# Optimization experiments

Hardware: AMD Instinct MI355X
Metric: run time of the kernel (lower is better)

The kernel has to match this reference:

```python
import jax, jax.numpy as jnp
import numpy as np
import math

B, T = 512, 512
ENC = 512          # 2 * input_size
N_MELS, R = 80, 2
ATTN, DEC = 256, 256
PRE_H, PRE_O = 256, 256
HID = 128          # DCA hidden
SC, SK = 8, 21     # static channels / kernel
DC, DK = 8, 21     # dynamic channels / kernel
PL, PA, PB = 11, 0.1, 0.9  # prior length, alpha, beta


def _betabinom_pmf(k, n, a, b):
    lg = math.lgamma
    return math.exp(lg(n + 1) - lg(k + 1) - lg(n - k + 1)
                    + lg(k + a) + lg(n - k + b) - lg(n + a + b)
                    - (lg(a) + lg(b) - lg(a + b)))


def setup_inputs() -> dict:
    key = jax.random.key(0)
    ks = iter(jax.random.split(key, 64))
    def rn(shape, s=0.05):
        return jax.random.normal(next(ks), shape, dtype=jnp.float32) * s
    inp = {}
    inp["h"] = rn([B, T, ENC], 1.0)
    inp["y"] = rn([B, N_MELS], 1.0)
    a = jax.random.uniform(next(ks), [B, T], dtype=jnp.float32)
    inp["alpha"] = a / a.sum(-1, keepdims=True)  # valid attention distribution
    inp["c"] = rn([B, ENC], 1.0)
    for n in ["attn_h0", "attn_c0", "rnn1_h0", "rnn1_c0", "rnn2_h0", "rnn2_c0"]:
        inp[n] = rn([B, ATTN], 1.0)
    # prenet
    inp["fc1_w"] = rn([PRE_H, N_MELS]); inp["fc1_b"] = rn([PRE_H])
    inp["fc2_w"] = rn([PRE_O, PRE_H]); inp["fc2_b"] = rn([PRE_O])
    # dynamic convolution attention
    inp["W_w"] = rn([HID, ATTN]); inp["W_b"] = rn([HID])
    inp["V_w"] = rn([DC * DK, HID])
    inp["F_w"] = rn([SC, 1, SK])
    inp["U_w"] = rn([HID, SC])
    inp["T_w"] = rn([HID, DC]); inp["T_b"] = rn([HID])
    inp["v_w"] = rn([1, HID])
    P = np.array([_betabinom_pmf(k, PL - 1, PA, PB) for k in range(PL)], np.float32)[::-1].copy()
    inp["P"] = jnp.asarray(P)
    # attn LSTM cell: input = 2*input_size + prenet output = 768
    inp["attn_wih"] = rn([4 * ATTN, ENC + PRE_O]); inp["attn_whh"] = rn([4 * ATTN, ATTN])
    inp["attn_bih"] = rn([4 * ATTN]); inp["attn_bhh"] = rn([4 * ATTN])
    inp["lin_w"] = rn([DEC, ENC + ATTN]); inp["lin_b"] = rn([DEC])
    for pfx in ["r1", "r2"]:
        inp[pfx + "_wih"] = rn([4 * DEC, DEC]); inp[pfx + "_whh"] = rn([4 * DEC, DEC])
        inp[pfx + "_bih"] = rn([4 * DEC]); inp[pfx + "_bhh"] = rn([4 * DEC])
    inp["proj_w"] = rn([N_MELS * R, DEC])
    return inp


def _lstm(x, h, c, wih, whh, bih, bhh):
    g = x @ wih.T + bih + h @ whh.T + bhh
    i, f, gg, o = jnp.split(g, 4, axis=-1)
    c2 = jax.nn.sigmoid(f) * c + jax.nn.sigmoid(i) * jnp.tanh(gg)
    return jax.nn.sigmoid(o) * jnp.tanh(c2), c2


def _win(x, k):
    # x: [B, T + k - 1] padded signal -> sliding windows [B, T, k]
    idx = jnp.arange(T)[:, None] + jnp.arange(k)[None, :]
    return x[:, idx]


def reference(h, y, alpha, c, attn_h0, attn_c0, rnn1_h0, rnn1_c0, rnn2_h0, rnn2_c0,
              fc1_w, fc1_b, fc2_w, fc2_b, W_w, W_b, V_w, F_w, U_w, T_w, T_b, v_w, P,
              attn_wih, attn_whh, attn_bih, attn_bhh, lin_w, lin_b,
              r1_wih, r1_whh, r1_bih, r1_bhh, r2_wih, r2_whh, r2_bih, r2_bhh, proj_w):
    # prenet (eval mode -> dropout inactive since fixed=False)
    yp = jax.nn.relu(jax.nn.relu(y @ fc1_w.T + fc1_b) @ fc2_w.T + fc2_b)
    attn_h, attn_c = _lstm(jnp.concatenate([c, yp], -1), attn_h0, attn_c0,
                           attn_wih, attn_whh, attn_bih, attn_bhh)
    # --- dynamic convolution attention ---
    # prior: causal conv with flipped beta-binomial pmf
    p = jnp.einsum('btk,k->bt', _win(jnp.pad(alpha, ((0, 0), (PL - 1, 0))), PL), P)
    p = jnp.log(jnp.clip(p, 1e-6))
    # dynamic filters per batch element: [B, DC, DK]
    G = (jnp.tanh(attn_h @ W_w.T + W_b) @ V_w.T).reshape(-1, DC, DK)
    wd = _win(jnp.pad(alpha, ((0, 0), ((DK - 1) // 2, (DK - 1) // 2))), DK)  # [B,T,DK]
    g = jnp.einsum('btk,bck->btc', wd, G)  # grouped conv1d, groups=B
    ws = _win(jnp.pad(alpha, ((0, 0), ((SK - 1) // 2, (SK - 1) // 2))), SK)
    f = jnp.einsum('btk,ck->btc', ws, F_w[:, 0, :])  # static conv1d
    e = jnp.squeeze(jnp.tanh(f @ U_w.T + g @ T_w.T + T_b) @ v_w.T, -1) + p
    alpha2 = jax.nn.softmax(e, axis=-1)
    # --- context + decoder stack ---
    c2 = jnp.einsum('bt,btd->bd', alpha2, h)
    x = jnp.concatenate([c2, attn_h], -1) @ lin_w.T + lin_b
    r1_h, r1_c = _lstm(x, rnn1_h0, rnn1_c0, r1_wih, r1_whh, r1_bih, r1_bhh)
    x = x + r1_h
    r2_h, r2_c = _lstm(x, rnn2_h0, rnn2_c0, r2_wih, r2_whh, r2_bih, r2_bhh)
    x = x + r2_h
    out = (x @ proj_w.T).reshape(-1, N_MELS, R)
    return (out, alpha2, c2, attn_h, attn_c, r1_h, r1_c, r2_h, r2_c)
```

## Files before the change

### kernel.cpp

```cpp
#include <hip/hip_runtime.h>

typedef unsigned short u16;
typedef __attribute__((ext_vector_type(8))) short s8v;
typedef __attribute__((ext_vector_type(4))) float f32x4;

__device__ __forceinline__ float bf2f(u16 u) { return __uint_as_float(((unsigned)u) << 16); }
__device__ __forceinline__ u16 f2bf(float f) {
    unsigned u = __float_as_uint(f);
    return (u16)((u + 0x7fffu + ((u >> 16) & 1u)) >> 16);
}
__device__ __forceinline__ float ldraw(const void* p, size_t i, int dt) {
    return dt ? ((const float*)p)[i] : bf2f(((const u16*)p)[i]);
}
__device__ __forceinline__ int fl(const int* F, int f) {
    return f == -1 ? 1 : (f == -2 ? 0 : F[f]);
}
__device__ __forceinline__ float fast_tanh(float x) {
    x = fminf(fmaxf(x, -15.f), 15.f);
    float e = __expf(2.f * x);
    return (e - 1.f) / (e + 1.f);
}
__device__ __forceinline__ float sigm(float x) { return 1.f / (1.f + __expf(-x)); }

__global__ __launch_bounds__(256) void k_detect(int* __restrict__ flagsRaw,
    const void* p0, const void* p1, const void* p2, const void* p3, const void* p4,
    const void* p5, const void* p6, const void* p7, const void* p8, const void* p9,
    const void* p10, const void* p11, const void* p12, const void* p13, const void* p14,
    const void* p15, const void* p16, const void* p17, const void* p18, const void* p19,
    const void* p20, const void* p21, const void* p22, const void* p23, const void* p24,
    const void* p25, const void* p26, const void* p27, const void* p28, const void* p29,
    const void* p30, const void* p31, const void* p32, const void* p33, const void* p34,
    const void* p35, const void* p36, const void* p37)
{
    const void* ptrs[38] = {p0,p1,p2,p3,p4,p5,p6,p7,p8,p9,p10,p11,p12,p13,p14,p15,p16,
                            p17,p18,p19,p20,p21,p22,p23,p24,p25,p26,p27,p28,p29,p30,p31,
                            p32,p33,p34,p35,p36,p37};
    const int ns[38] = {134217728, 40960, 262144, 262144,
                        131072,131072,131072,131072,131072,131072,
                        20480,256,65536,256,
                        32768,128,21504,168,1024,1024,128,128,11,
                        786432,262144,1024,1024, 196608,256,
                        262144,262144,1024,1024, 262144,262144,1024,1024, 40960};
    __shared__ int s;
    int b = blockIdx.x, tid = threadIdx.x;
    if (tid == 0) s = 0;
    __syncthreads();
    int nsamp = ns[b] >> 1;
    if (nsamp > 512) nsamp = 512;
    const u16* q = (const u16*)ptrs[b];
    int bad = 0;
    for (int i = tid; i < nsamp; i += 256) {
        u16 u = q[2 * i];
        int e = (u >> 7) & 0xff;
        bad += (e < 96 || e > 159) ? 1 : 0;
    }
    atomicAdd(&s, bad);
    __syncthreads();
    if (tid == 0) flagsRaw[b] = (s * 4 > nsamp) ? 1 : 0;
}

__global__ __launch_bounds__(256) void k_finish(
    const int* __restrict__ FRAW, int* __restrict__ FF,
    const void* a_wih, const void* a_whh, const void* r1_wih, const void* r1_whh,
    const void* r2_wih, const void* r2_whh,
    const void* U_w, const void* T_w, const void* T_b, const void* v_w, const void* F_w,
    u16* wihA, u16* whhA, u16* w1i, u16* w1h, u16* w2i, u16* w2h,
    float* utw, float* tbf, float* vf, float* ff)
{
    __shared__ int sflag[38];
    const int big[38] = {1,1,1,1, 1,1,1,1,1,1, 1,0,1,0,
                         1,0,1,0,1,1,0,0,0, 1,1,1,1, 1,0,
                         1,1,1,1, 1,1,1,1, 1};
    int tid = threadIdx.x;
    if (tid == 0) {
        int s = 0, c = 0;
        for (int i = 0; i < 38; i++) if (big[i]) { s += FRAW[i]; c++; }
        int maj = (s * 2 > c) ? 1 : 0;
        for (int i = 0; i < 38; i++) sflag[i] = big[i] ? FRAW[i] : maj;
        if (blockIdx.x == 0)
            for (int i = 0; i < 38; i++) FF[i] = sflag[i];
    }
    __syncthreads();

    if (blockIdx.x == 0) {
        int dU = sflag[18], dT = sflag[19], dTb = sflag[20], dV = sflag[21], dF = sflag[17];
        for (int i = tid; i < 1024; i += 256) {
            int j = i >> 3, c = i & 7;
            utw[j * 16 + c]     = ldraw(U_w, i, dU);
            utw[j * 16 + 8 + c] = ldraw(T_w, i, dT);
        }
        if (tid < 128) { tbf[tid] = ldraw(T_b, tid, dTb); vf[tid] = ldraw(v_w, tid, dV); }
        if (tid < 168) ff[tid] = ldraw(F_w, tid, dF);
    }

    const void* srcs[6] = {a_wih, a_whh, r1_wih, r1_whh, r2_wih, r2_whh};
    u16* dsts[6] = {wihA, whhA, w1i, w1h, w2i, w2h};
    const int nsg[6] = {786432, 262144, 262144, 262144, 262144, 262144};
    const int fsg[6] = {23, 24, 29, 30, 33, 34};
    int gtid = blockIdx.x * 256 + tid;
    int gstride = 2048 * 256;
    #pragma unroll
    for (int sgi = 0; sgi < 6; sgi++) {
        int nq = nsg[sgi] >> 2;
        int dt = sflag[fsg[sgi]];
        u16* dst = dsts[sgi];
        if (dt) {
            const float4* src = (const float4*)srcs[sgi];
            for (int q = gtid; q < nq; q += gstride) {
                float4 v = src[q];
                ushort4 o;
                o.x = f2bf(v.x); o.y = f2bf(v.y); o.z = f2bf(v.z); o.w = f2bf(v.w);
                *(ushort4*)&dst[q * 4] = o;
            }
        } else {
            const ushort4* src = (const ushort4*)srcs[sgi];
            for (int q = gtid; q < nq; q += gstride)
                *(ushort4*)&dst[q * 4] = src[q];
        }
    }
}

__device__ __forceinline__ void vg32_pair(const int* F,
    const void* A, int lda, int fa, const void* B, int ldb, int bo, int fb, int K,
    int m0, int n0, int N, int tid, int tx, int ty, float* acc,
    float (*As)[68], float (*Bs)[68])
{
    int dA = fl(F, fa), dB = fl(F, fb);
    bool fastp = dA && dB;
    for (int k0 = 0; k0 < K; k0 += 64) {
        __syncthreads();
        if (fastp) {
            #pragma unroll
            for (int p = 0; p < 2; p++) {
                int e = tid + p * 256;
                int row = e >> 4, kk = (e & 15) * 4;
                float4 va = {0.f, 0.f, 0.f, 0.f};
                if (k0 + kk < K)
                    va = *(const float4*)((const float*)A + (size_t)(m0 + row) * lda + k0 + kk);
                *(float4*)&As[row][kk] = va;
                int nr = n0 + row;
                float4 vb = {0.f, 0.f, 0.f, 0.f};
                if (nr < N && k0 + kk < K)
                    vb = *(const float4*)((const float*)B + (size_t)nr * ldb + bo + k0 + kk);
                *(float4*)&Bs[row][kk] = vb;
            }
        } else {
            #pragma unroll
            for (int p = 0; p < 8; p++) {
                int e = tid + p * 256;
                int row = e >> 6, kk = e & 63;
                As[row][kk] = (k0 + kk < K) ? ldraw(A, (size_t)(m0 + row) * lda + k0 + kk, dA) : 0.f;
                int nr = n0 + row;
                Bs[row][kk] = (nr < N && k0 + kk < K)
                            ? ldraw(B, (size_t)nr * ldb + bo + k0 + kk, dB) : 0.f;
            }
        }
        __syncthreads();
        #pragma unroll
        for (int kq = 0; kq < 16; kq++) {
            float4 a0 = *(const float4*)&As[ty][kq * 4];
            float4 a1 = *(const float4*)&As[ty + 16][kq * 4];
            float4 b0 = *(const float4*)&Bs[tx][kq * 4];
            float4 b1 = *(const float4*)&Bs[tx + 16][kq * 4];
            acc[0] += a0.x*b0.x + a0.y*b0.y + a0.z*b0.z + a0.w*b0.w;
            acc[1] += a0.x*b1.x + a0.y*b1.y + a0.z*b1.z + a0.w*b1.w;
            acc[2] += a1.x*b0.x + a1.y*b0.y + a1.z*b0.z + a1.w*b0.w;
            acc[3] += a1.x*b1.x + a1.y*b1.y + a1.z*b1.z + a1.w*b1.w;
        }
    }
}

__global__ __launch_bounds__(256) void k_vgemm32(
    const int* __restrict__ F,
    const void* A1, int lda1, int fa1, const void* B1, int ldb1, int bo1, int fb1, int K1,
    const void* A2, int lda2, int fa2, const void* B2, int ldb2, int bo2, int fb2, int K2,
    const void* bias1, int fx1,
    float* __restrict__ Cf, int ldc, int N, int act)
{
    __shared__ float As[32][68], Bs[32][68];
    int tid = threadIdx.x, tx = tid & 15, ty = tid >> 4;
    int m0 = blockIdx.y * 32, n0 = blockIdx.x * 32;
    float acc[4] = {0.f, 0.f, 0.f, 0.f};
    vg32_pair(F, A1, lda1, fa1, B1, ldb1, bo1, fb1, K1, m0, n0, N, tid, tx, ty, acc, As, Bs);
    if (A2) vg32_pair(F, A2, lda2, fa2, B2, ldb2, bo2, fb2, K2, m0, n0, N, tid, tx, ty, acc, As, Bs);

    #pragma unroll
    for (int c = 0; c < 2; c++) {
        int n = n0 + tx + c * 16;
        if (n >= N) continue;
        float bias = 0.f;
        if (bias1) bias += ldraw(bias1, n, fl(F, fx1));
        #pragma unroll
        for (int r = 0; r < 2; r++) {
            float v = acc[r * 2 + c] + bias;
            if (act == 1) v = fmaxf(v, 0.f);
            else if (act == 2) v = fast_tanh(v);
            Cf[(size_t)(m0 + ty + r * 16) * ldc + n] = v;
        }
    }
}

__global__ __launch_bounds__(256) void k_lin(
    const int* __restrict__ F, const float* __restrict__ part, float* __restrict__ o_c2,
    const float* __restrict__ ah, const void* lin_w, const void* lin_b,
    float* __restrict__ x1f)
{
    __shared__ float As[32][68], Bs[32][68];
    int tid = threadIdx.x, tx = tid & 15, ty = tid >> 4;
    int m0 = blockIdx.y * 32, n0 = blockIdx.x * 32;
    int dB = fl(F, 27);
    float acc[4] = {0.f, 0.f, 0.f, 0.f};
    for (int k0 = 0; k0 < 512; k0 += 64) {
        __syncthreads();
        #pragma unroll
        for (int p = 0; p < 2; p++) {
            int e = tid + p * 256;
            int row = e >> 4, kk = (e & 15) * 4;
            size_t idx = (size_t)(m0 + row) * 512 + k0 + kk;
            float4 va = *(const float4*)(part + idx);
            float4 vb2 = *(const float4*)(part + idx + 262144);
            va.x += vb2.x; va.y += vb2.y; va.z += vb2.z; va.w += vb2.w;
            *(float4*)&As[row][kk] = va;
            if (blockIdx.x == 0) *(float4*)(o_c2 + idx) = va;
            int nr = n0 + row;
            float4 vb;
            if (dB) {
                vb = *(const float4*)((const float*)lin_w + (size_t)nr * 768 + k0 + kk);
            } else {
                const u16* q = (const u16*)lin_w + (size_t)nr * 768 + k0 + kk;
                vb.x = bf2f(q[0]); vb.y = bf2f(q[1]); vb.z = bf2f(q[2]); vb.w = bf2f(q[3]);
            }
            *(float4*)&Bs[row][kk] = vb;
        }
        __syncthreads();
        #pragma unroll
        for (int kq = 0; kq < 16; kq++) {
            float4 a0 = *(const float4*)&As[ty][kq * 4];
            float4 a1 = *(const float4*)&As[ty + 16][kq * 4];
            float4 b0 = *(const float4*)&Bs[tx][kq * 4];
            float4 b1 = *(const float4*)&Bs[tx + 16][kq * 4];
            acc[0] += a0.x*b0.x + a0.y*b0.y + a0.z*b0.z + a0.w*b0.w;
            acc[1] += a0.x*b1.x + a0.y*b1.y + a0.z*b1.z + a0.w*b1.w;
            acc[2] += a1.x*b0.x + a1.y*b0.y + a1.z*b0.z + a1.w*b0.w;
            acc[3] += a1.x*b1.x + a1.y*b1.y + a1.z*b1.z + a1.w*b1.w;
        }
    }
    vg32_pair(F, ah, 256, -1, lin_w, 768, 512, 27, 256, m0, n0, 256, tid, tx, ty, acc, As, Bs);

    int dbias = fl(F, 28);
    #pragma unroll
    for (int c = 0; c < 2; c++) {
        int n = n0 + tx + c * 16;
        float bias = ldraw(lin_b, n, dbias);
        #pragma unroll
        for (int r = 0; r < 2; r++)
            x1f[(size_t)(m0 + ty + r * 16) * 256 + n] = acc[r * 2 + c] + bias;
    }
}

__device__ __forceinline__ void lstm_mfma_piece(const int* F,
    const void* A, int lda, int fa, const void* B, int ldb, int bo, int fb, int K,
    int b0, int j0, int tid, int wave, int lane, f32x4& acc,
    u16 (*As)[72], u16 (*Bs)[72])
{
    int dA = fl(F, fa), dB = fl(F, fb);
    for (int k0 = 0; k0 < K; k0 += 64) {
        __syncthreads();
        for (int g = tid; g < 640; g += 256) {
            const void* src; int dt; size_t idx; u16* dst;
            if (g < 128) {
                int row = g >> 3, kg = (g & 7) * 8;
                idx = (size_t)(b0 + row) * lda + k0 + kg;
                src = A; dt = dA; dst = &As[row][kg];
            } else {
                int gb = g - 128;
                int row = gb >> 3, kg = (gb & 7) * 8;
                int grow = (row >> 4) * 256 + j0 + (row & 15);
                idx = (size_t)grow * ldb + bo + k0 + kg;
                src = B; dt = dB; dst = &Bs[row][kg];
            }
            if (dt) {
                const float* sp = (const float*)src + idx;
                float4 a = *(const float4*)sp;
                float4 b = *(const float4*)(sp + 4);
                s8v v;
                v[0] = (short)f2bf(a.x); v[1] = (short)f2bf(a.y);
                v[2] = (short)f2bf(a.z); v[3] = (short)f2bf(a.w);
                v[4] = (short)f2bf(b.x); v[5] = (short)f2bf(b.y);
                v[6] = (short)f2bf(b.z); v[7] = (short)f2bf(b.w);
                *(s8v*)dst = v;
            } else {
                *(s8v*)dst = *(const s8v*)((const u16*)src + idx);
            }
        }
        __syncthreads();
        int r = lane & 15, kg = (lane >> 4) * 8;
        s8v a0 = *(const s8v*)&As[r][kg];
        s8v w0 = *(const s8v*)&Bs[wave * 16 + r][kg];
        acc = __builtin_amdgcn_mfma_f32_16x16x32_bf16(a0, w0, acc, 0, 0, 0);
        s8v a1 = *(const s8v*)&As[r][32 + kg];
        s8v w1 = *(const s8v*)&Bs[wave * 16 + r][32 + kg];
        acc = __builtin_amdgcn_mfma_f32_16x16x32_bf16(a1, w1, acc, 0, 0, 0);
    }
}

__global__ __launch_bounds__(256) void k_lstm(
    const int* __restrict__ F,
    const void* A1, int lda1, int fa1, const void* B1, int ldb1, int bo1, int fb1, int K1,
    const void* A2, int lda2, int fa2, const void* B2, int ldb2, int bo2, int fb2, int K2,
    const void* A3, int lda3, int fa3, const void* B3, int ldb3, int bo3, int fb3, int K3,
    const void* bih, int fx1, const void* bhh, int fx2,
    const void* c0, int fc0,
    float* __restrict__ h_out, float* __restrict__ c_out,
    const float* __restrict__ xprev, float* __restrict__ xout)
{
    __shared__ u16 As[16][72];
    __shared__ u16 Bs[64][72];
    __shared__ float sG[4][16][16];
    int tid = threadIdx.x, lane = tid & 63, wave = tid >> 6;
    int j0 = blockIdx.x * 16, b0 = blockIdx.y * 16;
    f32x4 acc = {0.f, 0.f, 0.f, 0.f};
    lstm_mfma_piece(F, A1, lda1, fa1, B1, ldb1, bo1, fb1, K1, b0, j0, tid, wave, lane, acc, As, Bs);
    if (A2) lstm_mfma_piece(F, A2, lda2, fa2, B2, ldb2, bo2, fb2, K2, b0, j0, tid, wave, lane, acc, As, Bs);
    if (A3) lstm_mfma_piece(F, A3, lda3, fa3, B3, ldb3, bo3, fb3, K3, b0, j0, tid, wave, lane, acc, As, Bs);

    #pragma unroll
    for (int r2 = 0; r2 < 4; r2++)
        sG[wave][(lane >> 4) * 4 + r2][lane & 15] = acc[r2];
    __syncthreads();

    int jl = tid & 15, bl = tid >> 4;
    int j = j0 + jl, b = b0 + bl;
    int dx1 = fl(F, fx1), dx2 = fl(F, fx2);
    float gi = sG[0][bl][jl] + ldraw(bih, j, dx1)       + ldraw(bhh, j, dx2);
    float gf = sG[1][bl][jl] + ldraw(bih, j + 256, dx1) + ldraw(bhh, j + 256, dx2);
    float gg = sG[2][bl][jl] + ldraw(bih, j + 512, dx1) + ldraw(bhh, j + 512, dx2);
    float go = sG[3][bl][jl] + ldraw(bih, j + 768, dx1) + ldraw(bhh, j + 768, dx2);
    size_t idx = (size_t)b * 256 + j;
    float cp = ldraw(c0, idx, F[fc0]);
    float cn = sigm(gf) * cp + sigm(gi) * fast_tanh(gg);
    float hn = sigm(go) * fast_tanh(cn);
    h_out[idx] = hn;
    c_out[idx] = cn;
    if (xprev) xout[idx] = xprev[idx] + hn;
}

__global__ __launch_bounds__(256) void k_dca(
    const int* __restrict__ F, const void* __restrict__ alpha, const void* __restrict__ P,
    const float* __restrict__ G, const float* __restrict__ utw, const float* __restrict__ tbf,
    const float* __restrict__ vf, const float* __restrict__ ff,
    float* __restrict__ o_a2)
{
    __shared__ float sFC[16][512];
    __shared__ float sal[532];
    __shared__ float spv[512];
    __shared__ float se[512];
    __shared__ float sff[168], sgd[168];
    __shared__ float sred[8];
    int dA = F[2], dP = F[22];
    int b = blockIdx.x, tid = threadIdx.x;
    if (tid < 168) { sff[tid] = ff[tid]; sgd[tid] = G[(size_t)b * 168 + tid]; }
    for (int i = tid; i < 532; i += 256)
        sal[i] = (i >= 10 && i < 522) ? ldraw(alpha, (size_t)b * 512 + i - 10, dA) : 0.f;
    float pfv[11];
    #pragma unroll
    for (int k = 0; k < 11; k++) pfv[k] = ldraw(P, k, dP);
    __syncthreads();

    #pragma unroll
    for (int q = 0; q < 2; q++) {
        int t = tid + q * 256;
        float aw[21];
        #pragma unroll
        for (int k = 0; k < 21; k++) aw[k] = sal[t + k];
        float pv = 0.f;
        #pragma unroll
        for (int k = 0; k < 11; k++) pv += aw[k] * pfv[k];
        spv[t] = pv;
        #pragma unroll
        for (int c = 0; c < 8; c++) {
            float s1 = 0.f, s2 = 0.f;
            #pragma unroll
            for (int k = 0; k < 21; k++) {
                s1 += aw[k] * sff[c * 21 + k];
                s2 += aw[k] * sgd[c * 21 + k];
            }
            sFC[c][t] = s1;
            sFC[8 + c][t] = s2;
        }
    }
    __syncthreads();

    int js = tid & 31, tg = tid >> 5;
    float4 uu[16];
    {
        const float4* up = (const float4*)(utw + js * 64);
        #pragma unroll
        for (int r = 0; r < 16; r++) uu[r] = up[r];
    }
    float tb4[4], v4[4];
    #pragma unroll
    for (int r = 0; r < 4; r++) { tb4[r] = tbf[js * 4 + r]; v4[r] = vf[js * 4 + r]; }

    for (int tt = 0; tt < 64; tt++) {
        int t = tg * 64 + tt;
        float fc2[8], gc2[8];
        #pragma unroll
        for (int c = 0; c < 8; c++) { fc2[c] = sFC[c][t]; gc2[c] = sFC[8 + c][t]; }
        float ep = 0.f;
        #pragma unroll
        for (int r = 0; r < 4; r++) {
            float4 u0 = uu[r * 4 + 0], u1 = uu[r * 4 + 1];
            float4 t0 = uu[r * 4 + 2], t1 = uu[r * 4 + 3];
            float a = tb4[r];
            a += fc2[0]*u0.x + fc2[1]*u0.y + fc2[2]*u0.z + fc2[3]*u0.w;
            a += fc2[4]*u1.x + fc2[5]*u1.y + fc2[6]*u1.z + fc2[7]*u1.w;
            a += gc2[0]*t0.x + gc2[1]*t0.y + gc2[2]*t0.z + gc2[3]*t0.w;
            a += gc2[4]*t1.x + gc2[5]*t1.y + gc2[6]*t1.z + gc2[7]*t1.w;
            ep += fast_tanh(a) * v4[r];
        }
        #pragma unroll
        for (int off = 16; off >= 1; off >>= 1) ep += __shfl_xor(ep, off);
        if (js == 0) se[t] = ep;
    }
    __syncthreads();

    float e0 = se[tid]       + __logf(fmaxf(spv[tid], 1e-6f));
    float e1 = se[tid + 256] + __logf(fmaxf(spv[tid + 256], 1e-6f));
    float m = fmaxf(e0, e1);
    #pragma unroll
    for (int off = 32; off >= 1; off >>= 1) m = fmaxf(m, __shfl_xor(m, off));
    if ((tid & 63) == 0) sred[tid >> 6] = m;
    __syncthreads();
    m = fmaxf(fmaxf(sred[0], sred[1]), fmaxf(sred[2], sred[3]));
    float x0 = __expf(e0 - m), x1 = __expf(e1 - m);
    float s = x0 + x1;
    #pragma unroll
    for (int off = 32; off >= 1; off >>= 1) s += __shfl_xor(s, off);
    if ((tid & 63) == 0) sred[4 + (tid >> 6)] = s;
    __syncthreads();
    s = sred[4] + sred[5] + sred[6] + sred[7];
    float inv = 1.f / s;
    o_a2[(size_t)b * 512 + tid]       = x0 * inv;
    o_a2[(size_t)b * 512 + tid + 256] = x1 * inv;
}

__global__ __launch_bounds__(256) void k_c2_part(
    const int* __restrict__ F, const float* __restrict__ a2,
    const void* __restrict__ h, float* __restrict__ part)
{
    int dH = F[0];
    int bi = blockIdx.x;
    int b = bi >> 1, sp = bi & 1;
    int tid = threadIdx.x;
    int dsub = (tid & 63) * 8;
    int tsub = tid >> 6;
    __shared__ float sa[256];
    sa[tid] = a2[(size_t)b * 512 + sp * 256 + tid];
    __syncthreads();
    float acc[8];
    #pragma unroll
    for (int j = 0; j < 8; j++) acc[j] = 0.f;
    size_t rowbase = (size_t)b * 512 + sp * 256;
    if (dH) {
        const float* hf = (const float*)h;
        for (int tt = tsub; tt < 256; tt += 4) {
            float a = sa[tt];
            const float* p = hf + (rowbase + tt) * 512 + dsub;
            float4 v0 = *(const float4*)p, v1 = *(const float4*)(p + 4);
            acc[0] += a * v0.x; acc[1] += a * v0.y; acc[2] += a * v0.z; acc[3] += a * v0.w;
            acc[4] += a * v1.x; acc[5] += a * v1.y; acc[6] += a * v1.z; acc[7] += a * v1.w;
        }
    } else {
        const u16* hb = (const u16*)h;
        for (int tt = tsub; tt < 256; tt += 4) {
            float a = sa[tt];
            const u16* p = hb + (rowbase + tt) * 512 + dsub;
            #pragma unroll
            for (int j = 0; j < 8; j++) acc[j] += a * bf2f(p[j]);
        }
    }
    __shared__ float sacc[256 * 8];
    #pragma unroll
    for (int j = 0; j < 8; j++) sacc[tid * 8 + j] = acc[j];
    __syncthreads();
    if (tid < 64) {
        float* pp = part + ((size_t)sp * 512 + b) * 512 + tid * 8;
        #pragma unroll
        for (int j = 0; j < 8; j++)
            pp[j] = sacc[tid * 8 + j] + sacc[(tid + 64) * 8 + j]
                  + sacc[(tid + 128) * 8 + j] + sacc[(tid + 192) * 8 + j];
    }
}

__global__ void k_plant_direct(float* out0, float v) {
    if (threadIdx.x == 0 && blockIdx.x == 0) out0[0] = v;
}

extern "C" void kernel_launch(void* const* d_in, const int* in_sizes, int n_in,
                              void* d_out, int out_size, void* d_ws, size_t ws_size,
                              hipStream_t stream)
{
    (void)out_size; (void)ws_size;
    float* outf = (float*)d_out;

    static const int exp_sizes[38] = {
        134217728, 40960, 262144, 262144,
        131072,131072,131072,131072,131072,131072,
        20480,256,65536,256,
        32768,128,21504,168,1024,1024,128,128,11,
        786432,262144,1024,1024, 196608,256,
        262144,262144,1024,1024, 262144,262144,1024,1024, 40960};
    int bad = 0;
    if (n_in != 38) bad = 100;
    else for (int i = 0; i < 38; i++)
        if (in_sizes[i] != exp_sizes[i]) { bad = i + 1; break; }
    if (bad) {
        k_plant_direct<<<1, 1, 0, stream>>>(outf, 4194304.f + 65536.f * (float)bad);
        return;
    }

    const void* h_enc  = d_in[0];  const void* y      = d_in[1];
    const void* alpha  = d_in[2];  const void* c_in   = d_in[3];
    const void* ah0    = d_in[4];  const void* ac0    = d_in[5];
    const void* r1h0   = d_in[6];  const void* r1c0   = d_in[7];
    const void* r2h0   = d_in[8];  const void* r2c0   = d_in[9];
    const void* fc1_w  = d_in[10]; const void* fc1_b  = d_in[11];
    const void* fc2_w  = d_in[12]; const void* fc2_b  = d_in[13];
    const void* W_w    = d_in[14]; const void* W_b    = d_in[15];
    const void* V_w    = d_in[16]; const void* F_w    = d_in[17];
    const void* U_w    = d_in[18]; const void* T_w    = d_in[19];
    const void* T_b    = d_in[20]; const void* v_w    = d_in[21];
    const void* P      = d_in[22];
    const void* a_wih  = d_in[23]; const void* a_whh  = d_in[24];
    const void* a_bih  = d_in[25]; const void* a_bhh  = d_in[26];
    const void* lin_w  = d_in[27]; const void* lin_b  = d_in[28];
    const void* r1_wih = d_in[29]; const void* r1_whh = d_in[30];
    const void* r1_bih = d_in[31]; const void* r1_bhh = d_in[32];
    const void* r2_wih = d_in[33]; const void* r2_whh = d_in[34];
    const void* r2_bih = d_in[35]; const void* r2_bhh = d_in[36];
    const void* proj_w = d_in[37];

    char* ws = (char*)d_ws;
    int*   FRAW = (int*)  (ws + 0);
    int*   FF   = (int*)  (ws + 256);
    float* utw  = (float*)(ws + 1024);
    float* tbf  = (float*)(ws + 9216);
    float* vf   = (float*)(ws + 9728);
    float* ffs  = (float*)(ws + 10240);
    float* h1f  = (float*)(ws + 12288);
    float* ypf  = (float*)(ws + 536576);
    float* thf  = (float*)(ws + 1060864);
    float* Gdf  = (float*)(ws + 1323008);
    float* part = (float*)(ws + 1667072);
    u16*   wihA = (u16*)  (ws + 3764224);
    u16*   whhA = (u16*)  (ws + 5337088);
    u16*   w1i  = (u16*)  (ws + 5861376);
    u16*   w1h  = (u16*)  (ws + 6385664);
    u16*   w2i  = (u16*)  (ws + 6909952);
    u16*   w2h  = (u16*)  (ws + 7434240);

    float* o_out = outf + 0;
    float* o_a2  = outf + 81920;
    float* o_c2  = outf + 344064;
    float* o_ah  = outf + 606208;
    float* o_ac  = outf + 737280;
    float* o_r1h = outf + 868352;
    float* o_r1c = outf + 999424;
    float* o_r2h = outf + 1130496;
    float* o_r2c = outf + 1261568;

    const void* nv = nullptr;
    dim3 blk(256, 1, 1);

    k_detect<<<38, blk, 0, stream>>>(FRAW,
        d_in[0], d_in[1], d_in[2], d_in[3], d_in[4], d_in[5], d_in[6], d_in[7], d_in[8],
        d_in[9], d_in[10], d_in[11], d_in[12], d_in[13], d_in[14], d_in[15], d_in[16],
        d_in[17], d_in[18], d_in[19], d_in[20], d_in[21], d_in[22], d_in[23], d_in[24],
        d_in[25], d_in[26], d_in[27], d_in[28], d_in[29], d_in[30], d_in[31], d_in[32],
        d_in[33], d_in[34], d_in[35], d_in[36], d_in[37]);
    k_finish<<<2048, blk, 0, stream>>>(FRAW, FF,
        a_wih, a_whh, r1_wih, r1_whh, r2_wih, r2_whh,
        U_w, T_w, T_b, v_w, F_w,
        wihA, whhA, w1i, w1h, w2i, w2h, utw, tbf, vf, ffs);

    k_vgemm32<<<dim3(8, 16), blk, 0, stream>>>(FF,
        y, 80, 1, fc1_w, 80, 0, 10, 80,
        nv, 0, -1, nv, 0, 0, -1, 0,
        fc1_b, 11, h1f, 256, 256, 1);
    k_vgemm32<<<dim3(8, 16), blk, 0, stream>>>(FF,
        h1f, 256, -1, fc2_w, 256, 0, 12, 256,
        nv, 0, -1, nv, 0, 0, -1, 0,
        fc2_b, 13, ypf, 256, 256, 1);

    k_lstm<<<dim3(16, 32), blk, 0, stream>>>(FF,
        c_in, 512, 3, wihA, 768, 0, -2, 512,
        ypf, 256, -1, wihA, 768, 512, -2, 256,
        ah0, 256, 4, whhA, 256, 0, -2, 256,
        a_bih, 25, a_bhh, 26, ac0, 5, o_ah, o_ac, nullptr, nullptr);

    k_vgemm32<<<dim3(4, 16), blk, 0, stream>>>(FF,
        o_ah, 256, -1, W_w, 256, 0, 14, 256,
        nv, 0, -1, nv, 0, 0, -1, 0,
        W_b, 15, thf, 128, 128, 2);
    k_vgemm32<<<dim3(6, 16), blk, 0, stream>>>(FF,
        thf, 128, -1, V_w, 128, 0, 16, 128,
        nv, 0, -1, nv, 0, 0, -1, 0,
        nv, -1, Gdf, 168, 168, 0);

    k_dca<<<512, blk, 0, stream>>>(FF, alpha, P, Gdf, utw, tbf, vf, ffs, o_a2);

    k_c2_part<<<1024, blk, 0, stream>>>(FF, o_a2, h_enc, part);

    float* x1f = h1f;
    float* x2f = ypf;
    k_lin<<<dim3(8, 16), blk, 0, stream>>>(FF, part, o_c2, o_ah, lin_w, lin_b, x1f);

    k_lstm<<<dim3(16, 32), blk, 0, stream>>>(FF,
        x1f, 256, -1, w1i, 256, 0, -2, 256,
        r1h0, 256, 6, w1h, 256, 0, -2, 256,
        nv, 0, -1, nv, 0, 0, -1, 0,
        r1_bih, 31, r1_bhh, 32, r1c0, 7, o_r1h, o_r1c, x1f, x2f);

    float* x3f = h1f;
    k_lstm<<<dim3(16, 32), blk, 0, stream>>>(FF,
        x2f, 256, -1, w2i, 256, 0, -2, 256,
        r2h0, 256, 8, w2h, 256, 0, -2, 256,
        nv, 0, -1, nv, 0, 0, -1, 0,
        r2_bih, 35, r2_bhh, 36, r2c0, 9, o_r2h, o_r2c, x2f, x3f);

    k_vgemm32<<<dim3(5, 16), blk, 0, stream>>>(FF,
        x3f, 256, -1, proj_w, 256, 0, 37, 256,
        nv, 0, -1, nv, 0, 0, -1, 0,
        nv, -1, o_out, 160, 160, 0);
}
```

Measured before the change: 324.6 us.

## Fuse prenet and DCA filter GEMM pairs into single kernels via LDS intermediates

Replaces the two back-to-back prenet GEMM launches (fc1+relu, fc2+relu) with one kernel that keeps the 32-row hidden activations in shared memory. It does the same for the W/tanh and V GEMMs that produce the dynamic filters. This removes two kernel launches and the global round trips of the intermediate buffers, and the workspace layout is compacted to match. In exchange each fused kernel runs on only 16 blocks and loops serially over the output tiles, so far less of the GPU is used per launch.

```diff
diff --git a/kernel.cpp b/kernel.cpp
--- a/kernel.cpp
+++ b/kernel.cpp
@@ -197,6 +197,123 @@
             else if (act == 2) v = fast_tanh(v);
             Cf[(size_t)(m0 + ty + r * 16) * ldc + n] = v;
         }
+    }
+}
+
+template<int LDSA>
+__device__ __forceinline__ void lds_pair(const int* F,
+    const float (*sA)[LDSA], const void* B, int ldb, int fb, int K,
+    int n0, int N, int tid, int tx, int ty, float* acc, float (*Bs)[68])
+{
+    int dB = fl(F, fb);
+    for (int k0 = 0; k0 < K; k0 += 64) {
+        __syncthreads();
+        if (dB) {
+            #pragma unroll
+            for (int p = 0; p < 2; p++) {
+                int e = tid + p * 256;
+                int row = e >> 4, kk = (e & 15) * 4;
+                int nr = n0 + row;
+                float4 vb = {0.f, 0.f, 0.f, 0.f};
+                if (nr < N)
+                    vb = *(const float4*)((const float*)B + (size_t)nr * ldb + k0 + kk);
+                *(float4*)&Bs[row][kk] = vb;
+            }
+        } else {
+            #pragma unroll
+            for (int p = 0; p < 8; p++) {
+                int e = tid + p * 256;
+                int row = e >> 6, kk = e & 63;
+                int nr = n0 + row;
+                Bs[row][kk] = (nr < N) ? bf2f(((const u16*)B)[(size_t)nr * ldb + k0 + kk]) : 0.f;
+            }
+        }
+        __syncthreads();
+        #pragma unroll
+        for (int kq = 0; kq < 16; kq++) {
+            float4 a0 = *(const float4*)&sA[ty][k0 + kq * 4];
+            float4 a1 = *(const float4*)&sA[ty + 16][k0 + kq * 4];
+            float4 b0 = *(const float4*)&Bs[tx][kq * 4];
+            float4 b1 = *(const float4*)&Bs[tx + 16][kq * 4];
+            acc[0] += a0.x*b0.x + a0.y*b0.y + a0.z*b0.z + a0.w*b0.w;
+            acc[1] += a0.x*b1.x + a0.y*b1.y + a0.z*b1.z + a0.w*b1.w;
+            acc[2] += a1.x*b0.x + a1.y*b0.y + a1.z*b0.z + a1.w*b0.w;
+            acc[3] += a1.x*b1.x + a1.y*b1.y + a1.z*b1.z + a1.w*b1.w;
+        }
+    }
+}
+
+__global__ __launch_bounds__(256) void k_pre(
+    const int* __restrict__ F, const void* y, const void* fc1_w, const void* fc1_b,
+    const void* fc2_w, const void* fc2_b, float* __restrict__ ypf)
+{
+    __shared__ float As[32][68], Bs[32][68];
+    __shared__ float sH[32][260];
+    int tid = threadIdx.x, tx = tid & 15, ty = tid >> 4;
+    int m0 = blockIdx.x * 32;
+    int d1b = fl(F, 11), d2b = fl(F, 13);
+    for (int nt = 0; nt < 8; nt++) {
+        float acc[4] = {0.f, 0.f, 0.f, 0.f};
+        vg32_pair(F, y, 80, 1, fc1_w, 80, 0, 10, 80, m0, nt * 32, 256, tid, tx, ty, acc, As, Bs);
+        #pragma unroll
+        for (int c = 0; c < 2; c++) {
+            int n = nt * 32 + tx + c * 16;
+            float bias = ldraw(fc1_b, n, d1b);
+            #pragma unroll
+            for (int r = 0; r < 2; r++)
+                sH[ty + r * 16][n] = fmaxf(acc[r * 2 + c] + bias, 0.f);
+        }
+    }
+    __syncthreads();
+    for (int nt = 0; nt < 8; nt++) {
+        float acc[4] = {0.f, 0.f, 0.f, 0.f};
+        lds_pair<260>(F, sH, fc2_w, 256, 12, 256, nt * 32, 256, tid, tx, ty, acc, Bs);
+        #pragma unroll
+        for (int c = 0; c < 2; c++) {
+            int n = nt * 32 + tx + c * 16;
+            float bias = ldraw(fc2_b, n, d2b);
+            #pragma unroll
+            for (int r = 0; r < 2; r++)
+                ypf[(size_t)(m0 + ty + r * 16) * 256 + n] = fmaxf(acc[r * 2 + c] + bias, 0.f);
+        }
+        __syncthreads();
+    }
+}
+
+__global__ __launch_bounds__(256) void k_wv(
+    const int* __restrict__ F, const float* __restrict__ ah,
+    const void* W_w, const void* W_b, const void* V_w, float* __restrict__ Gdf)
+{
+    __shared__ float As[32][68], Bs[32][68];
+    __shared__ float sTh[32][132];
+    int tid = threadIdx.x, tx = tid & 15, ty = tid >> 4;
+    int m0 = blockIdx.x * 32;
+    int dWb = fl(F, 15);
+    for (int nt = 0; nt < 4; nt++) {
+        float acc[4] = {0.f, 0.f, 0.f, 0.f};
+        vg32_pair(F, ah, 256, -1, W_w, 256, 0, 14, 256, m0, nt * 32, 128, tid, tx, ty, acc, As, Bs);
+        #pragma unroll
+        for (int c = 0; c < 2; c++) {
+            int n = nt * 32 + tx + c * 16;
+            float bias = ldraw(W_b, n, dWb);
+            #pragma unroll
+            for (int r = 0; r < 2; r++)
+                sTh[ty + r * 16][n] = fast_tanh(acc[r * 2 + c] + bias);
+        }
+    }
+    __syncthreads();
+    for (int nt = 0; nt < 6; nt++) {
+        float acc[4] = {0.f, 0.f, 0.f, 0.f};
+        lds_pair<132>(F, sTh, V_w, 128, 16, 128, nt * 32, 168, tid, tx, ty, acc, Bs);
+        #pragma unroll
+        for (int c = 0; c < 2; c++) {
+            int n = nt * 32 + tx + c * 16;
+            if (n >= 168) continue;
+            #pragma unroll
+            for (int r = 0; r < 2; r++)
+                Gdf[(size_t)(m0 + ty + r * 16) * 168 + n] = acc[r * 2 + c];
+        }
+        __syncthreads();
     }
 }
 
@@ -550,15 +667,14 @@
     float* ffs  = (float*)(ws + 10240);
     float* h1f  = (float*)(ws + 12288);
     float* ypf  = (float*)(ws + 536576);
-    float* thf  = (float*)(ws + 1060864);
-    float* Gdf  = (float*)(ws + 1323008);
-    float* part = (float*)(ws + 1667072);
-    u16*   wihA = (u16*)  (ws + 3764224);
-    u16*   whhA = (u16*)  (ws + 5337088);
-    u16*   w1i  = (u16*)  (ws + 5861376);
-    u16*   w1h  = (u16*)  (ws + 6385664);
-    u16*   w2i  = (u16*)  (ws + 6909952);
-    u16*   w2h  = (u16*)  (ws + 7434240);
+    float* Gdf  = (float*)(ws + 1060864);
+    float* part = (float*)(ws + 1404928);
+    u16*   wihA = (u16*)  (ws + 3502080);
+    u16*   whhA = (u16*)  (ws + 5074944);
+    u16*   w1i  = (u16*)  (ws + 5599232);
+    u16*   w1h  = (u16*)  (ws + 6123520);
+    u16*   w2i  = (u16*)  (ws + 6647808);
+    u16*   w2h  = (u16*)  (ws + 7172096);
 
     float* o_out = outf + 0;
     float* o_a2  = outf + 81920;
@@ -584,14 +700,7 @@
         U_w, T_w, T_b, v_w, F_w,
         wihA, whhA, w1i, w1h, w2i, w2h, utw, tbf, vf, ffs);
 
-    k_vgemm32<<<dim3(8, 16), blk, 0, stream>>>(FF,
-        y, 80, 1, fc1_w, 80, 0, 10, 80,
-        nv, 0, -1, nv, 0, 0, -1, 0,
-        fc1_b, 11, h1f, 256, 256, 1);
-    k_vgemm32<<<dim3(8, 16), blk, 0, stream>>>(FF,
-        h1f, 256, -1, fc2_w, 256, 0, 12, 256,
-        nv, 0, -1, nv, 0, 0, -1, 0,
-        fc2_b, 13, ypf, 256, 256, 1);
+    k_pre<<<16, blk, 0, stream>>>(FF, y, fc1_w, fc1_b, fc2_w, fc2_b, ypf);
 
     k_lstm<<<dim3(16, 32), blk, 0, stream>>>(FF,
         c_in, 512, 3, wihA, 768, 0, -2, 512,
@@ -599,14 +708,7 @@
         ah0, 256, 4, whhA, 256, 0, -2, 256,
         a_bih, 25, a_bhh, 26, ac0, 5, o_ah, o_ac, nullptr, nullptr);
 
-    k_vgemm32<<<dim3(4, 16), blk, 0, stream>>>(FF,
-        o_ah, 256, -1, W_w, 256, 0, 14, 256,
-        nv, 0, -1, nv, 0, 0, -1, 0,
-        W_b, 15, thf, 128, 128, 2);
-    k_vgemm32<<<dim3(6, 16), blk, 0, stream>>>(FF,
-        thf, 128, -1, V_w, 128, 0, 16, 128,
-        nv, 0, -1, nv, 0, 0, -1, 0,
-        nv, -1, Gdf, 168, 168, 0);
+    k_wv<<<16, blk, 0, stream>>>(FF, o_ah, W_w, W_b, V_w, Gdf);
 
     k_dca<<<512, blk, 0, stream>>>(FF, alpha, P, Gdf, utw, tbf, vf, ffs, o_a2);
 
```

Measured after the change: 495.7 us. +52.7%, slower.
